# Kernel tuning notes

Hardware: AMD Instinct MI355X
Metric: run time of the kernel (lower is better)

## Reference

```python
import jax, jax.numpy as jnp
import numpy as np


def setup_inputs() -> dict:
    key = jax.random.key(0)
    k1, k2, k3 = jax.random.split(key, 3)
    B, DIM, H, Wd = 32, 512, 64, 64
    K, DQ = 64, 3
    features = jax.random.normal(k1, (B, DIM, H, Wd), dtype=jnp.float32)
    query = jax.random.normal(k2, (B, DQ, H, Wd), dtype=jnp.float32)
    # Ensemble of K 1x1 convs (no bias): weight [K, dim_query, dim], scaled like conv init
    W = jax.random.normal(k3, (K, DQ, DIM), dtype=jnp.float32) * (1.0 / np.sqrt(DIM))
    return {"features": features, "query": query, "W": W}


def reference(features, query, W):
    B = query.shape[0]
    # ensemble 1x1 conv: key_values [k, b, q, h, w]
    kv = jnp.einsum('kqd,bdhw->kbqhw', W, features)
    # rearrange 'k b ... -> b k ...'
    kv_b = jnp.transpose(kv, (1, 0, 2, 3, 4))          # [b, k, q, h, w]
    q_flat = query.reshape(B, 1, -1)                    # [b, 1, N]
    kv_flat = kv_b.reshape(B, kv_b.shape[1], -1)        # [b, k, N]
    # torch.cdist (p=2) between [b,1,N] and [b,k,N] -> [b,k]
    diff = q_flat - kv_flat
    distance = jnp.sqrt(jnp.sum(diff * diff, axis=-1))  # [b, k]
    codes = jnp.argmin(distance, axis=-1)               # [b]
    # batched gather of selected key_values
    idx = codes[:, None, None, None, None]
    sel_key_values = jnp.take_along_axis(kv_b, idx, axis=1)[:, 0]  # [b, q, h, w]
    commit_loss = jnp.mean((sel_key_values - query) ** 2)
    return sel_key_values, codes, commit_loss
```

## Files before the change

### kernel.cpp

```cpp
#include <hip/hip_runtime.h>
#include <hip/hip_bf16.h>
#include <hip/hip_fp16.h>

#define BN   32
#define DIMK 512
#define HW   4096
#define KK   64
#define DQ   3
#define RR   192
#define NT   128
#define NBLK (HW / NT)

typedef _Float16 half8  __attribute__((ext_vector_type(8)));
typedef float    f32x4  __attribute__((ext_vector_type(4)));
typedef short    short8 __attribute__((ext_vector_type(8)));

#define A16_OFF    0
#define A16_BYTES  (RR * DIMK * 2)
#define DIST2_OFF  196608
#define DIST2_BYTES (BN * KK * 4)
#define KV_OFF     262144
#define KV_BYTES   ((size_t)BN * RR * HW * 2)

#define OUT_SEL    ((size_t)BN * DQ * HW)
#define OUT_LOSS   (OUT_SEL + BN)

__global__ void init_kernel(const float* __restrict__ Wsrc,
                            _Float16* __restrict__ A16,
                            float* __restrict__ dist2,
                            float* __restrict__ out) {
  int gid = blockIdx.x * 256 + threadIdx.x;
  if (gid < RR * DIMK) A16[gid] = (_Float16)Wsrc[gid];
  if (gid < BN * KK)   dist2[gid] = 0.f;
  if (gid == 0)        out[OUT_LOSS] = 0.f;
}

template <bool STORE>
__global__ __launch_bounds__(256) void gemm_dist_kernel(
    const float* __restrict__ f, const float* __restrict__ query,
    const _Float16* __restrict__ A16, __hip_bfloat16* __restrict__ kv,
    float* __restrict__ dist2) {
  __shared__ __align__(16) _Float16 Alds[2][RR][40];
  __shared__ __align__(16) _Float16 Blds[2][4][NT][8];
  __shared__ float qlds[DQ][NT];
  __shared__ float rowsum[RR];

  const int t  = threadIdx.x;
  const int w  = t >> 6;
  const int l  = t & 63;
  const int lq = l >> 4;
  const int ln = l & 15;
  const int b  = blockIdx.y;
  const int n0 = blockIdx.x * NT;

  for (int s = t; s < DQ * NT; s += 256) {
    int q = s / NT, n = s % NT;
    qlds[q][n] = query[((size_t)b * DQ + q) * HW + n0 + n];
  }

  f32x4 acc[3][8];
#pragma unroll
  for (int mt = 0; mt < 3; mt++)
#pragma unroll
    for (int nt = 0; nt < 8; nt++) acc[mt][nt] = (f32x4)0.f;

  const int bn  = t & (NT - 1);
  const int bkb = t >> 7;

  float bpre[16];
  half8 apre[3];

  auto loadTile = [&](int kk) {
    const float* fp = f + ((size_t)b * DIMK + kk * 32 + bkb * 16) * HW + n0 + bn;
#pragma unroll
    for (int j = 0; j < 16; j++) bpre[j] = fp[(size_t)j * HW];
#pragma unroll
    for (int i = 0; i < 3; i++) {
      int s = t + i * 256;
      int m = s >> 2, oct = s & 3;
      apre[i] = *(const half8*)&A16[m * DIMK + kk * 32 + oct * 8];
    }
  };
  auto stageTile = [&](int buf) {
#pragma unroll
    for (int i = 0; i < 3; i++) {
      int s = t + i * 256;
      int m = s >> 2, oct = s & 3;
      *(half8*)&Alds[buf][m][oct * 8] = apre[i];
    }
    half8 h0, h1;
#pragma unroll
    for (int j = 0; j < 8; j++) { h0[j] = (_Float16)bpre[j]; h1[j] = (_Float16)bpre[8 + j]; }
    *(half8*)&Blds[buf][2 * bkb][bn][0]     = h0;
    *(half8*)&Blds[buf][2 * bkb + 1][bn][0] = h1;
  };

  loadTile(0);
  stageTile(0);
  for (int kk = 0; kk < DIMK / 32; kk++) {
    const int cur = kk & 1;
    __syncthreads();
    if (kk < DIMK / 32 - 1) loadTile(kk + 1);

    half8 af[3], bf[8];
#pragma unroll
    for (int mt = 0; mt < 3; mt++)
      af[mt] = *(const half8*)&Alds[cur][w * 48 + mt * 16 + ln][lq * 8];
#pragma unroll
    for (int nt = 0; nt < 8; nt++)
      bf[nt] = *(const half8*)&Blds[cur][lq][nt * 16 + ln][0];
#pragma unroll
    for (int mt = 0; mt < 3; mt++)
#pragma unroll
      for (int nt = 0; nt < 8; nt++)
        acc[mt][nt] = __builtin_amdgcn_mfma_f32_16x16x32_f16(af[mt], bf[nt],
                                                             acc[mt][nt], 0, 0, 0);
    if (kk < DIMK / 32 - 1) stageTile(cur ^ 1);
  }

  float rs[3][4];
#pragma unroll
  for (int mt = 0; mt < 3; mt++)
#pragma unroll
    for (int i = 0; i < 4; i++) rs[mt][i] = 0.f;

#pragma unroll
  for (int mt = 0; mt < 3; mt++) {
#pragma unroll
    for (int i = 0; i < 4; i++) {
      int r = w * 48 + mt * 16 + lq * 4 + i;
      int q = r % 3;
#pragma unroll
      for (int nt = 0; nt < 8; nt++) {
        int n = nt * 16 + ln;
        float c = acc[mt][nt][i];
        if (STORE) kv[((size_t)b * RR + r) * HW + n0 + n] = __float2bfloat16(c);
        float d = c - qlds[q][n];
        rs[mt][i] += d * d;
      }
    }
  }
#pragma unroll
  for (int mt = 0; mt < 3; mt++)
#pragma unroll
    for (int i = 0; i < 4; i++) {
      float v = rs[mt][i];
      v += __shfl_xor(v, 1, 64);
      v += __shfl_xor(v, 2, 64);
      v += __shfl_xor(v, 4, 64);
      v += __shfl_xor(v, 8, 64);
      rs[mt][i] = v;
    }
  if (ln < 12) {
    int mt = ln >> 2, i = ln & 3;
    rowsum[w * 48 + mt * 16 + lq * 4 + i] = rs[mt][i];
  }
  __syncthreads();
  if (t < KK) {
    float v = rowsum[3 * t] + rowsum[3 * t + 1] + rowsum[3 * t + 2];
    atomicAdd(&dist2[b * KK + t], v);
  }
}

__global__ __launch_bounds__(256) void gather_kernel(
    const __hip_bfloat16* __restrict__ kv, const float* __restrict__ query,
    const float* __restrict__ dist2, float* __restrict__ out) {
  int b = blockIdx.x, t = threadIdx.x;
  __shared__ int scode;
  __shared__ float red[4];
  if (t == 0) {
    float best = dist2[b * KK]; int bi = 0;
    for (int k = 1; k < KK; k++) {
      float v = dist2[b * KK + k];
      if (v < best) { best = v; bi = k; }
    }
    scode = bi;
    out[OUT_SEL + b] = (float)bi;
  }
  __syncthreads();
  int code = scode;
  const short8* src = (const short8*)(kv + ((size_t)b * RR + code * DQ) * HW);
  const f32x4*  qp  = (const f32x4*)(query + (size_t)b * DQ * HW);
  f32x4*        op  = (f32x4*)(out + (size_t)b * DQ * HW);
  float lsum = 0.f;
  for (int c = t; c < DQ * HW / 8; c += 256) {
    short8 v = src[c];
    f32x4 o0, o1;
#pragma unroll
    for (int j = 0; j < 4; j++) {
      unsigned u0 = ((unsigned)(unsigned short)v[j]) << 16;
      unsigned u1 = ((unsigned)(unsigned short)v[4 + j]) << 16;
      o0[j] = __builtin_bit_cast(float, u0);
      o1[j] = __builtin_bit_cast(float, u1);
    }
    f32x4 q0 = qp[2 * c], q1 = qp[2 * c + 1];
    op[2 * c] = o0; op[2 * c + 1] = o1;
#pragma unroll
    for (int j = 0; j < 4; j++) {
      float d0 = o0[j] - q0[j], d1 = o1[j] - q1[j];
      lsum += d0 * d0 + d1 * d1;
    }
  }
  for (int off = 1; off < 64; off <<= 1) lsum += __shfl_xor(lsum, off, 64);
  if ((t & 63) == 0) red[t >> 6] = lsum;
  __syncthreads();
  if (t == 0)
    atomicAdd(&out[OUT_LOSS],
              (red[0] + red[1] + red[2] + red[3]) * (1.f / (float)(BN * DQ * HW)));
}

__global__ __launch_bounds__(256) void recompute_kernel(
    const float* __restrict__ f, const float* __restrict__ query,
    const float* __restrict__ Wsrc, const float* __restrict__ dist2,
    float* __restrict__ out) {
  int b = blockIdx.y, t = threadIdx.x;
  int hw = blockIdx.x * 256 + t;
  __shared__ int scode;
  __shared__ float red[4];
  if (t == 0) {
    float best = dist2[b * KK]; int bi = 0;
    for (int k = 1; k < KK; k++) {
      float v = dist2[b * KK + k];
      if (v < best) { best = v; bi = k; }
    }
    scode = bi;
    if (blockIdx.x == 0) out[OUT_SEL + b] = (float)bi;
  }
  __syncthreads();
  int code = scode;
  const float* w0 = Wsrc + (size_t)code * DQ * DIMK;
  const float* fp = f + (size_t)b * DIMK * HW + hw;
  float a0 = 0.f, a1 = 0.f, a2 = 0.f;
  for (int d = 0; d < DIMK; d++) {
    float fv = fp[(size_t)d * HW];
    a0 += w0[d] * fv;
    a1 += w0[DIMK + d] * fv;
    a2 += w0[2 * DIMK + d] * fv;
  }
  const float* qp = query + (size_t)b * DQ * HW;
  float* op = out + (size_t)b * DQ * HW;
  op[hw] = a0; op[HW + hw] = a1; op[2 * HW + hw] = a2;
  float d0 = a0 - qp[hw], d1 = a1 - qp[HW + hw], d2 = a2 - qp[2 * HW + hw];
  float lsum = d0 * d0 + d1 * d1 + d2 * d2;
  for (int off = 1; off < 64; off <<= 1) lsum += __shfl_xor(lsum, off, 64);
  if ((t & 63) == 0) red[t >> 6] = lsum;
  __syncthreads();
  if (t == 0)
    atomicAdd(&out[OUT_LOSS],
              (red[0] + red[1] + red[2] + red[3]) * (1.f / (float)(BN * DQ * HW)));
}

extern "C" void kernel_launch(void* const* d_in, const int* in_sizes, int n_in,
                              void* d_out, int out_size, void* d_ws, size_t ws_size,
                              hipStream_t stream) {
  const float* f     = (const float*)d_in[0];
  const float* query = (const float*)d_in[1];
  const float* Wsrc  = (const float*)d_in[2];
  float* out = (float*)d_out;
  char*  ws  = (char*)d_ws;

  _Float16*        A16   = (_Float16*)(ws + A16_OFF);
  float*           dist2 = (float*)(ws + DIST2_OFF);
  __hip_bfloat16*  kv    = (__hip_bfloat16*)(ws + KV_OFF);

  const bool store = ws_size >= (size_t)KV_OFF + KV_BYTES;

  init_kernel<<<384, 256, 0, stream>>>(Wsrc, A16, dist2, out);
  if (store) {
    gemm_dist_kernel<true><<<dim3(NBLK, BN), 256, 0, stream>>>(f, query, A16, kv, dist2);
    gather_kernel<<<BN, 256, 0, stream>>>(kv, query, dist2, out);
  } else {
    gemm_dist_kernel<false><<<dim3(NBLK, BN), 256, 0, stream>>>(f, query, A16, nullptr, dist2);
    recompute_kernel<<<dim3(HW / 256, BN), 256, 0, stream>>>(f, query, Wsrc, dist2, out);
  }
}
```

Baseline: 382.4 us.

## Pre-pad W tiles and load A via direct global-to-LDS; split gather across blocks

The init kernel now writes the fp16 weights in a per-k-slice padded layout. The GEMM then streams A tiles straight into LDS with global_load_lds, with no register staging. The MFMA loop loads B fragments in two groups of four, and launch bounds request 3 waves per SIMD, both to cut register pressure and raise occupancy. The gather kernel is split across 4 blocks per batch and uses a wave-level shuffle argmin, exposing more parallelism in the final pass. The risk is that direct-to-LDS loads and the new occupancy bound could cause spills or ordering issues. The shuffle argmin's tie-breaking also needs to match the sequential first-minimum rule.

```diff
diff --git a/kernel.cpp b/kernel.cpp
--- a/kernel.cpp
+++ b/kernel.cpp
@@ -10,14 +10,19 @@
 #define RR   192
 #define NT   128
 #define NBLK (HW / NT)
+#define NKK  (DIMK / 32)
+
+#define AP_ROW   40
+#define AP_SLICE (RR * AP_ROW)
 
 typedef _Float16 half8  __attribute__((ext_vector_type(8)));
+typedef _Float16 half4  __attribute__((ext_vector_type(4)));
 typedef float    f32x4  __attribute__((ext_vector_type(4)));
 typedef short    short8 __attribute__((ext_vector_type(8)));
 
-#define A16_OFF    0
-#define A16_BYTES  (RR * DIMK * 2)
-#define DIST2_OFF  196608
+#define AP_OFF     0
+#define AP_BYTES   (NKK * AP_SLICE * 2)
+#define DIST2_OFF  245760
 #define DIST2_BYTES (BN * KK * 4)
 #define KV_OFF     262144
 #define KV_BYTES   ((size_t)BN * RR * HW * 2)
@@ -26,21 +31,30 @@
 #define OUT_LOSS   (OUT_SEL + BN)
 
 __global__ void init_kernel(const float* __restrict__ Wsrc,
-                            _Float16* __restrict__ A16,
+                            _Float16* __restrict__ Ap,
                             float* __restrict__ dist2,
                             float* __restrict__ out) {
   int gid = blockIdx.x * 256 + threadIdx.x;
-  if (gid < RR * DIMK) A16[gid] = (_Float16)Wsrc[gid];
-  if (gid < BN * KK)   dist2[gid] = 0.f;
-  if (gid == 0)        out[OUT_LOSS] = 0.f;
+  int d4 = gid * 4;
+  if (d4 < RR * DIMK) {
+    f32x4 v = *(const f32x4*)&Wsrc[d4];
+    half4 h;
+#pragma unroll
+    for (int j = 0; j < 4; j++) h[j] = (_Float16)v[j];
+    int m = d4 >> 9;
+    int d = d4 & 511;
+    *(half4*)&Ap[((size_t)(d >> 5) * RR + m) * AP_ROW + (d & 31)] = h;
+  }
+  if (gid < BN * KK) dist2[gid] = 0.f;
+  if (gid == 0)      out[OUT_LOSS] = 0.f;
 }
 
 template <bool STORE>
-__global__ __launch_bounds__(256) void gemm_dist_kernel(
+__global__ __launch_bounds__(256, 3) void gemm_dist_kernel(
     const float* __restrict__ f, const float* __restrict__ query,
-    const _Float16* __restrict__ A16, __hip_bfloat16* __restrict__ kv,
+    const _Float16* __restrict__ Ap, __hip_bfloat16* __restrict__ kv,
     float* __restrict__ dist2) {
-  __shared__ __align__(16) _Float16 Alds[2][RR][40];
+  __shared__ __align__(16) _Float16 Alds[2][RR][AP_ROW];
   __shared__ __align__(16) _Float16 Blds[2][4][NT][8];
   __shared__ float qlds[DQ][NT];
   __shared__ float rowsum[RR];
@@ -66,56 +80,66 @@
 
   const int bn  = t & (NT - 1);
   const int bkb = t >> 7;
+  const float* fbase = f + ((size_t)b * DIMK + bkb * 16) * HW + n0 + bn;
 
   float bpre[16];
-  half8 apre[3];
 
   auto loadTile = [&](int kk) {
-    const float* fp = f + ((size_t)b * DIMK + kk * 32 + bkb * 16) * HW + n0 + bn;
+    const float* fp = fbase + (size_t)kk * 32 * HW;
 #pragma unroll
     for (int j = 0; j < 16; j++) bpre[j] = fp[(size_t)j * HW];
-#pragma unroll
-    for (int i = 0; i < 3; i++) {
-      int s = t + i * 256;
-      int m = s >> 2, oct = s & 3;
-      apre[i] = *(const half8*)&A16[m * DIMK + kk * 32 + oct * 8];
-    }
   };
   auto stageTile = [&](int buf) {
-#pragma unroll
-    for (int i = 0; i < 3; i++) {
-      int s = t + i * 256;
-      int m = s >> 2, oct = s & 3;
-      *(half8*)&Alds[buf][m][oct * 8] = apre[i];
-    }
     half8 h0, h1;
 #pragma unroll
     for (int j = 0; j < 8; j++) { h0[j] = (_Float16)bpre[j]; h1[j] = (_Float16)bpre[8 + j]; }
     *(half8*)&Blds[buf][2 * bkb][bn][0]     = h0;
     *(half8*)&Blds[buf][2 * bkb + 1][bn][0] = h1;
   };
+  auto stageA = [&](int kk, int buf) {
+    const char* gs = (const char*)Ap + (size_t)kk * (AP_SLICE * 2) + (size_t)l * 16;
+    char* ls = (char*)&Alds[buf][0][0];
+#pragma unroll
+    for (int jj = 0; jj < 4; jj++) {
+      int i = w + 4 * jj;
+      if (jj < 3 || w < 3) {
+        __builtin_amdgcn_global_load_lds(
+            (const __attribute__((address_space(1))) unsigned int*)(const void*)(gs + i * 1024),
+            (__attribute__((address_space(3))) unsigned int*)(void*)(ls + i * 1024),
+            16, 0, 0);
+      }
+    }
+  };
 
   loadTile(0);
+  stageA(0, 0);
   stageTile(0);
-  for (int kk = 0; kk < DIMK / 32; kk++) {
+  for (int kk = 0; kk < NKK; kk++) {
     const int cur = kk & 1;
     __syncthreads();
-    if (kk < DIMK / 32 - 1) loadTile(kk + 1);
-
-    half8 af[3], bf[8];
+    if (kk < NKK - 1) {
+      loadTile(kk + 1);
+      stageA(kk + 1, cur ^ 1);
+    }
+
+    half8 af[3];
 #pragma unroll
     for (int mt = 0; mt < 3; mt++)
       af[mt] = *(const half8*)&Alds[cur][w * 48 + mt * 16 + ln][lq * 8];
 #pragma unroll
-    for (int nt = 0; nt < 8; nt++)
-      bf[nt] = *(const half8*)&Blds[cur][lq][nt * 16 + ln][0];
-#pragma unroll
-    for (int mt = 0; mt < 3; mt++)
-#pragma unroll
-      for (int nt = 0; nt < 8; nt++)
-        acc[mt][nt] = __builtin_amdgcn_mfma_f32_16x16x32_f16(af[mt], bf[nt],
-                                                             acc[mt][nt], 0, 0, 0);
-    if (kk < DIMK / 32 - 1) stageTile(cur ^ 1);
+    for (int g = 0; g < 2; g++) {
+      half8 bf[4];
+#pragma unroll
+      for (int nt = 0; nt < 4; nt++)
+        bf[nt] = *(const half8*)&Blds[cur][lq][(g * 4 + nt) * 16 + ln][0];
+#pragma unroll
+      for (int mt = 0; mt < 3; mt++)
+#pragma unroll
+        for (int nt = 0; nt < 4; nt++)
+          acc[mt][g * 4 + nt] = __builtin_amdgcn_mfma_f32_16x16x32_f16(
+              af[mt], bf[nt], acc[mt][g * 4 + nt], 0, 0, 0);
+    }
+    if (kk < NKK - 1) stageTile(cur ^ 1);
   }
 
   float rs[3][4];
@@ -165,17 +189,22 @@
 __global__ __launch_bounds__(256) void gather_kernel(
     const __hip_bfloat16* __restrict__ kv, const float* __restrict__ query,
     const float* __restrict__ dist2, float* __restrict__ out) {
-  int b = blockIdx.x, t = threadIdx.x;
+  int b = blockIdx.y, t = threadIdx.x;
   __shared__ int scode;
   __shared__ float red[4];
-  if (t == 0) {
-    float best = dist2[b * KK]; int bi = 0;
-    for (int k = 1; k < KK; k++) {
-      float v = dist2[b * KK + k];
-      if (v < best) { best = v; bi = k; }
-    }
-    scode = bi;
-    out[OUT_SEL + b] = (float)bi;
+  if (t < 64) {
+    float v = dist2[b * KK + t];
+    int idx = t;
+#pragma unroll
+    for (int off = 1; off < 64; off <<= 1) {
+      float ov = __shfl_xor(v, off, 64);
+      int   oi = __shfl_xor(idx, off, 64);
+      if (ov < v || (ov == v && oi < idx)) { v = ov; idx = oi; }
+    }
+    if (t == 0) {
+      scode = idx;
+      if (blockIdx.x == 0) out[OUT_SEL + b] = (float)idx;
+    }
   }
   __syncthreads();
   int code = scode;
@@ -183,7 +212,8 @@
   const f32x4*  qp  = (const f32x4*)(query + (size_t)b * DQ * HW);
   f32x4*        op  = (f32x4*)(out + (size_t)b * DQ * HW);
   float lsum = 0.f;
-  for (int c = t; c < DQ * HW / 8; c += 256) {
+  const int c0 = blockIdx.x * 384;
+  for (int c = c0 + t; c < c0 + 384; c += 256) {
     short8 v = src[c];
     f32x4 o0, o1;
 #pragma unroll
@@ -259,18 +289,18 @@
   float* out = (float*)d_out;
   char*  ws  = (char*)d_ws;
 
-  _Float16*        A16   = (_Float16*)(ws + A16_OFF);
+  _Float16*        Ap    = (_Float16*)(ws + AP_OFF);
   float*           dist2 = (float*)(ws + DIST2_OFF);
   __hip_bfloat16*  kv    = (__hip_bfloat16*)(ws + KV_OFF);
 
   const bool store = ws_size >= (size_t)KV_OFF + KV_BYTES;
 
-  init_kernel<<<384, 256, 0, stream>>>(Wsrc, A16, dist2, out);
+  init_kernel<<<96, 256, 0, stream>>>(Wsrc, Ap, dist2, out);
   if (store) {
-    gemm_dist_kernel<true><<<dim3(NBLK, BN), 256, 0, stream>>>(f, query, A16, kv, dist2);
-    gather_kernel<<<BN, 256, 0, stream>>>(kv, query, dist2, out);
+    gemm_dist_kernel<true><<<dim3(NBLK, BN), 256, 0, stream>>>(f, query, Ap, kv, dist2);
+    gather_kernel<<<dim3(4, BN), 256, 0, stream>>>(kv, query, dist2, out);
   } else {
-    gemm_dist_kernel<false><<<dim3(NBLK, BN), 256, 0, stream>>>(f, query, A16, nullptr, dist2);
+    gemm_dist_kernel<false><<<dim3(NBLK, BN), 256, 0, stream>>>(f, query, Ap, nullptr, dist2);
     recompute_kernel<<<dim3(HW / 256, BN), 256, 0, stream>>>(f, query, Wsrc, dist2, out);
   }
 }
```

After: 381.5 us. No clear change (-0.2%).
